# Performance work log

Measured on AMD Instinct MI355X. Metric: run time of the kernel, lower is better.

## Reference

```python
import jax, jax.numpy as jnp
import numpy as np

B, T = 32, 256
CHAR_V, BICHAR_V, CTYPE_V = 10000, 200000, 8
CD, BD, TD = 100, 100, 20
LIN, H = 200, 200
IN_DIMS = 2 * CD + 2 * BD + TD  # 420


def lstm_scan(xs, Wih, Whh, b, reverse=False):
    # xs: [T, B, LIN]; Wih: [4H, LIN]; Whh: [4H, H]; b: [4H]
    h0 = jnp.zeros((xs.shape[1], Whh.shape[1]), xs.dtype)
    c0 = jnp.zeros_like(h0)

    def step(carry, x):
        h, c = carry
        g = x @ Wih.T + h @ Whh.T + b  # [B, 4H]
        i, f, gg, o = jnp.split(g, 4, axis=-1)  # torch LSTMCell gate order
        c = jax.nn.sigmoid(f) * c + jax.nn.sigmoid(i) * jnp.tanh(gg)
        h = jax.nn.sigmoid(o) * jnp.tanh(c)
        return (h, c), h

    _, hs = jax.lax.scan(step, (h0, c0), xs, reverse=reverse)
    return hs  # [T, B, H]


def setup_inputs() -> dict:
    key = jax.random.key(0)
    ks = jax.random.split(key, 20)
    d = {
        "chars": jax.random.randint(ks[0], (B, T), 0, CHAR_V, jnp.int32),
        "left_bichar": jax.random.randint(ks[1], (B, T), 0, BICHAR_V, jnp.int32),
        "right_bichar": jax.random.randint(ks[2], (B, T), 0, BICHAR_V, jnp.int32),
        "extchars": jax.random.randint(ks[3], (B, T), 0, CHAR_V, jnp.int32),
        "extleft_bichar": jax.random.randint(ks[4], (B, T), 0, BICHAR_V, jnp.int32),
        "extright_bichar": jax.random.randint(ks[5], (B, T), 0, BICHAR_V, jnp.int32),
        "char_type": jax.random.randint(ks[6], (B, T), 0, CTYPE_V, jnp.int32),
        "E_char": jax.random.normal(ks[7], (CHAR_V, CD), jnp.float32) * 0.1,
        "E_extchar": jax.random.normal(ks[8], (CHAR_V, CD), jnp.float32) * 0.1,
        "E_bichar": jax.random.normal(ks[9], (BICHAR_V, BD), jnp.float32) * 0.1,
        "E_extbichar": jax.random.normal(ks[10], (BICHAR_V, BD), jnp.float32) * 0.1,
        "E_ctype": jax.random.normal(ks[11], (CTYPE_V, TD), jnp.float32) * 0.1,
        "fc_w": jax.random.normal(ks[12], (LIN, IN_DIMS), jnp.float32) * (1.0 / np.sqrt(IN_DIMS)),
        "fc_b": jnp.zeros((LIN,), jnp.float32),
        "Wih_l": jax.random.normal(ks[13], (4 * H, LIN), jnp.float32) * (1.0 / np.sqrt(LIN)),
        "Whh_l": jax.random.normal(ks[14], (4 * H, H), jnp.float32) * (1.0 / np.sqrt(H)),
        "b_l": jnp.zeros((4 * H,), jnp.float32),
        "Wih_r": jax.random.normal(ks[15], (4 * H, LIN), jnp.float32) * (1.0 / np.sqrt(LIN)),
        "Whh_r": jax.random.normal(ks[16], (4 * H, H), jnp.float32) * (1.0 / np.sqrt(H)),
        "b_r": jnp.zeros((4 * H,), jnp.float32),
    }
    return d


def reference(chars, left_bichar, right_bichar, extchars, extleft_bichar,
              extright_bichar, char_type, E_char, E_extchar, E_bichar,
              E_extbichar, E_ctype, fc_w, fc_b, Wih_l, Whh_l, b_l,
              Wih_r, Whh_r, b_r):
    c_e = E_char[chars]            # [B,T,CD]
    ec_e = E_extchar[extchars]
    lb_e = E_bichar[left_bichar]   # [B,T,BD]
    elb_e = E_extbichar[extleft_bichar]
    rb_e = E_bichar[right_bichar]
    erb_e = E_extbichar[extright_bichar]
    ct_e = E_ctype[char_type]      # [B,T,TD]

    left_total = jnp.concatenate([c_e, ec_e, lb_e, elb_e, ct_e], axis=2)
    right_total = jnp.concatenate([c_e, ec_e, rb_e, erb_e, ct_e], axis=2)

    left_x = jnp.tanh(left_total @ fc_w.T + fc_b).transpose(1, 0, 2)   # [T,B,LIN]
    right_x = jnp.tanh(right_total @ fc_w.T + fc_b).transpose(1, 0, 2)

    left_hs = lstm_scan(left_x, Wih_l, Whh_l, b_l, reverse=False)   # [T,B,H]
    right_hs = lstm_scan(right_x, Wih_r, Whh_r, b_r, reverse=True)  # [T,B,H]

    out = jnp.concatenate([left_hs, right_hs], axis=2).transpose(1, 0, 2)  # [B,T,2H]
    return out
```

## Files before the change

### kernel.cpp

```cpp
#include <hip/hip_runtime.h>
#include <stdint.h>

#define B_    32
#define T_    256
#define CD    100
#define BD    100
#define TD    20
#define LIN   200
#define HD    200
#define INDIM 420
#define G4    800

typedef __attribute__((ext_vector_type(8))) short bfrag8;
typedef __attribute__((ext_vector_type(4))) float f32x4v;

static __device__ __forceinline__ unsigned short f2bf(float f) {
  unsigned u = __float_as_uint(f);
  u = u + 0x7fffu + ((u >> 16) & 1u);
  return (unsigned short)(u >> 16);
}
static __device__ __forceinline__ float bf2f(unsigned short s) {
  return __uint_as_float(((unsigned)s) << 16);
}
static __device__ __forceinline__ float tanhx(float x) {
  return 1.0f - 2.0f * __builtin_amdgcn_rcpf(1.0f + __builtin_amdgcn_exp2f(x * 2.8853900817779268f));
}
static __device__ __forceinline__ float clamp40(float x) {
  return fminf(fmaxf(x, -40.0f), 40.0f);
}

static __device__ __forceinline__ void mk_hilo(float4 a, float4 b, bfrag8& hi, bfrag8& lo) {
  float q[8] = {a.x, a.y, a.z, a.w, b.x, b.y, b.z, b.w};
  #pragma unroll
  for (int j = 0; j < 8; ++j) {
    unsigned short h = f2bf(q[j]);
    hi[j] = (short)h;
    lo[j] = (short)f2bf(q[j] - bf2f(h));
  }
}
static __device__ __forceinline__ bfrag8 mk_hi(float4 a, float4 b) {
  bfrag8 r;
  float q[8] = {a.x, a.y, a.z, a.w, b.x, b.y, b.z, b.w};
  #pragma unroll
  for (int j = 0; j < 8; ++j) r[j] = (short)f2bf(q[j]);
  return r;
}

__global__ void presplit_kernel(const float* __restrict__ fc_w,
                                const float* __restrict__ Wih_l,
                                const float* __restrict__ Wih_r,
                                unsigned short* __restrict__ fcw_hi,
                                unsigned short* __restrict__ fcw_lo,
                                unsigned short* __restrict__ wih_hi,
                                unsigned short* __restrict__ wih_lo) {
  int tid = blockIdx.x * blockDim.x + threadIdx.x;
  int stride = gridDim.x * blockDim.x;
  for (int i = tid; i < 13 * 14 * 512; i += stride) {
    int j = i & 7, l = (i >> 3) & 63, f = i >> 9;
    int kt = f % 14, nt = f / 14;
    int n = nt * 16 + (l & 15);
    int k = kt * 32 + ((l >> 4) << 3) + j;
    float v = (n < LIN && k < INDIM) ? fc_w[n * INDIM + k] : 0.0f;
    unsigned short h = f2bf(v);
    fcw_hi[i] = h;
    fcw_lo[i] = f2bf(v - bf2f(h));
  }
  for (int d = 0; d < 2; ++d) {
    const float* W = d ? Wih_r : Wih_l;
    unsigned short* oh = wih_hi + (size_t)d * 179200;
    unsigned short* ol = wih_lo + (size_t)d * 179200;
    for (int i = tid; i < 50 * 7 * 512; i += stride) {
      int j = i & 7, l = (i >> 3) & 63, f = i >> 9;
      int kt = f % 7, nt = f / 7;
      int np = nt * 16 + (l & 15);
      int no = (np & 3) * 200 + (np >> 2);
      int k = kt * 32 + ((l >> 4) << 3) + j;
      float v = (k < LIN) ? W[no * LIN + k] : 0.0f;
      unsigned short h = f2bf(v);
      oh[i] = h;
      ol[i] = f2bf(v - bf2f(h));
    }
  }
}

__global__ __launch_bounds__(256) void fc_kernel(
    const int* __restrict__ chars, const int* __restrict__ left_bichar,
    const int* __restrict__ right_bichar, const int* __restrict__ extchars,
    const int* __restrict__ extleft, const int* __restrict__ extright,
    const int* __restrict__ ctype,
    const float* __restrict__ E_char, const float* __restrict__ E_extchar,
    const float* __restrict__ E_bichar, const float* __restrict__ E_extbichar,
    const float* __restrict__ E_ctype, const float* __restrict__ fc_b,
    const unsigned short* __restrict__ fcw_hi, const unsigned short* __restrict__ fcw_lo,
    float* __restrict__ x) {
  __shared__ __align__(16) float feat[32 * 452];
  int rb = blockIdx.x;
  int dir = rb >> 8;
  int t = rb & 255;
  int tid = threadIdx.x;
  const int* bi  = dir ? right_bichar : left_bichar;
  const int* ebi = dir ? extright : extleft;

  for (int cc = tid; cc < 32 * 113; cc += 256) {
    int lr = cc / 113, kc = cc - lr * 113;
    int k = kc << 2;
    float4 v = make_float4(0.f, 0.f, 0.f, 0.f);
    if (k < INDIM) {
      int id; const float* tab; int kk; int wdt;
      if (k < 100)      { id = chars[lr * T_ + t];    tab = E_char;      kk = k;       wdt = 100; }
      else if (k < 200) { id = extchars[lr * T_ + t]; tab = E_extchar;   kk = k - 100; wdt = 100; }
      else if (k < 300) { id = bi[lr * T_ + t];       tab = E_bichar;    kk = k - 200; wdt = 100; }
      else if (k < 400) { id = ebi[lr * T_ + t];      tab = E_extbichar; kk = k - 300; wdt = 100; }
      else              { id = ctype[lr * T_ + t];    tab = E_ctype;     kk = k - 400; wdt = 20;  }
      v = *reinterpret_cast<const float4*>(tab + (size_t)id * wdt + kk);
    }
    *reinterpret_cast<float4*>(&feat[lr * 452 + k]) = v;
  }
  __syncthreads();

  int w = tid >> 6, l = tid & 63;
  int lrow = l & 15, lk8 = (l >> 4) << 3;
  f32x4v acc[8];
  #pragma unroll
  for (int i = 0; i < 8; ++i) acc[i] = (f32x4v){0.f, 0.f, 0.f, 0.f};

  for (int kt = 0; kt < 14; ++kt) {
    bfrag8 ah[2], al[2];
    #pragma unroll
    for (int mt = 0; mt < 2; ++mt) {
      const float* fp = &feat[(mt * 16 + lrow) * 452 + kt * 32 + lk8];
      float4 v0 = *reinterpret_cast<const float4*>(fp);
      float4 v1 = *reinterpret_cast<const float4*>(fp + 4);
      mk_hilo(v0, v1, ah[mt], al[mt]);
    }
    #pragma unroll
    for (int s = 0; s < 4; ++s) {
      int nt = w + (s << 2);
      if (nt < 13) {
        size_t fo = ((size_t)(nt * 14 + kt) * 64 + l) * 8;
        bfrag8 bh = *reinterpret_cast<const bfrag8*>(fcw_hi + fo);
        bfrag8 bl = *reinterpret_cast<const bfrag8*>(fcw_lo + fo);
        #pragma unroll
        for (int mt = 0; mt < 2; ++mt) {
          acc[s * 2 + mt] = __builtin_amdgcn_mfma_f32_16x16x32_bf16(ah[mt], bh, acc[s * 2 + mt], 0, 0, 0);
          acc[s * 2 + mt] = __builtin_amdgcn_mfma_f32_16x16x32_bf16(al[mt], bh, acc[s * 2 + mt], 0, 0, 0);
          acc[s * 2 + mt] = __builtin_amdgcn_mfma_f32_16x16x32_bf16(ah[mt], bl, acc[s * 2 + mt], 0, 0, 0);
        }
      }
    }
  }
  int r0 = rb * 32;
  #pragma unroll
  for (int s = 0; s < 4; ++s) {
    int nt = w + (s << 2);
    if (nt < 13) {
      int n = nt * 16 + lrow;
      if (n < LIN) {
        float bias = fc_b[n];
        #pragma unroll
        for (int mt = 0; mt < 2; ++mt) {
          #pragma unroll
          for (int rr = 0; rr < 4; ++rr) {
            int row = mt * 16 + ((l >> 4) << 2) + rr;
            x[(size_t)(r0 + row) * LIN + n] = tanhx(acc[s * 2 + mt][rr] + bias);
          }
        }
      }
    }
  }
}

__global__ __launch_bounds__(512) void xwih_kernel(
    const float* __restrict__ x, const unsigned short* __restrict__ wih_hi,
    const unsigned short* __restrict__ wih_lo, const float* __restrict__ b_l,
    const float* __restrict__ b_r, float* __restrict__ pre) {
  int bid = blockIdx.x;
  int dir = (bid >= 320) ? 1 : 0;
  int rem = bid - dir * 320;
  int rbm = rem / 5, nb = rem - rbm * 5;
  int m0 = rbm * 128, n0 = nb * 160;
  int tid = threadIdx.x, w = tid >> 6, l = tid & 63;
  int lrow = l & 15, lk8 = (l >> 4) << 3;
  const float* xd = x + (size_t)dir * 8192 * LIN;
  const unsigned short* wh = wih_hi + (size_t)dir * 179200;
  const unsigned short* wl = wih_lo + (size_t)dir * 179200;
  const float* bias = dir ? b_r : b_l;

  f32x4v acc[10];
  #pragma unroll
  for (int i = 0; i < 10; ++i) acc[i] = (f32x4v){0.f, 0.f, 0.f, 0.f};

  int row = m0 + w * 16 + lrow;
  for (int kt = 0; kt < 7; ++kt) {
    int kb = kt * 32 + lk8;
    bfrag8 ah = {0,0,0,0,0,0,0,0}, al = {0,0,0,0,0,0,0,0};
    if (kb <= 192) {
      const float* fp = xd + (size_t)row * LIN + kb;
      float4 v0 = *reinterpret_cast<const float4*>(fp);
      float4 v1 = *reinterpret_cast<const float4*>(fp + 4);
      mk_hilo(v0, v1, ah, al);
    }
    #pragma unroll
    for (int nt = 0; nt < 10; ++nt) {
      int ntg = nb * 10 + nt;
      size_t fo = ((size_t)(ntg * 7 + kt) * 64 + l) * 8;
      bfrag8 bh = *reinterpret_cast<const bfrag8*>(wh + fo);
      bfrag8 bl = *reinterpret_cast<const bfrag8*>(wl + fo);
      acc[nt] = __builtin_amdgcn_mfma_f32_16x16x32_bf16(ah, bh, acc[nt], 0, 0, 0);
      acc[nt] = __builtin_amdgcn_mfma_f32_16x16x32_bf16(al, bh, acc[nt], 0, 0, 0);
      acc[nt] = __builtin_amdgcn_mfma_f32_16x16x32_bf16(ah, bl, acc[nt], 0, 0, 0);
    }
  }
  #pragma unroll
  for (int nt = 0; nt < 10; ++nt) {
    int n = n0 + nt * 16 + lrow;
    float bb = bias[(n & 3) * 200 + (n >> 2)];
    int hcol = n >> 2, g = n & 3;
    int i6 = hcol >> 5;
    int hc5 = hcol & 31;
    int wv = hc5 >> 2, lhi = hc5 & 3;
    int chunk = (i6 < 6) ? (i6 * 8 + wv) : (48 + wv);
    #pragma unroll
    for (int rr = 0; rr < 4; ++rr) {
      int r2 = m0 + w * 16 + ((l >> 4) << 2) + rr;
      int t = r2 >> 5, b32 = r2 & 31;
      int hf2 = b32 >> 4, b = b32 & 15;
      int lane = b + 16 * lhi;
      size_t dst = ((((size_t)(dir * 2 + hf2) * 256 + t) * 50 + chunk) * 64 + lane) * 4 + g;
      pre[dst] = acc[nt][rr] + bb;
    }
  }
}

__global__ __launch_bounds__(512, 2) void lstm_kernel(
    const float* __restrict__ pre, const float* __restrict__ Whh_l,
    const float* __restrict__ Whh_r, float* __restrict__ out) {
  __shared__ __align__(16) unsigned short hbufA[3584];
  __shared__ __align__(16) unsigned short hbufB[3584];
  __shared__ __align__(16) unsigned short whx[7168];
  __shared__ __align__(16) float pbuf0[12800];
  __shared__ __align__(16) float pbuf1[12800];

  int bi = blockIdx.x;
  int dir = bi >> 1, half = bi & 1;
  const float* Whh = dir ? Whh_r : Whh_l;
  int tid = threadIdx.x, w = tid >> 6, l = tid & 63;
  int lrow = l & 15, lk8 = (l >> 4) << 3;

  bfrag8 Breg[6][7];
  #pragma unroll
  for (int i = 0; i < 6; ++i) {
    int np = (w + 8 * i) * 16 + lrow;
    int no = (np & 3) * 200 + (np >> 2);
    #pragma unroll
    for (int kt = 0; kt < 7; ++kt) {
      int kb = kt * 32 + lk8;
      bfrag8 bb = {0,0,0,0,0,0,0,0};
      if (kb <= 192) {
        const float* fp = Whh + (size_t)no * HD + kb;
        bb = mk_hi(*reinterpret_cast<const float4*>(fp),
                   *reinterpret_cast<const float4*>(fp + 4));
      }
      Breg[i][kt] = bb;
    }
  }
  for (int e = tid; e < 896; e += 512) {
    int l2 = e & 63, f = e >> 6;
    int kt = f % 7, tile = f / 7;
    int np = (48 + tile) * 16 + (l2 & 15);
    int no = (np & 3) * 200 + (np >> 2);
    int kb = kt * 32 + ((l2 >> 4) << 3);
    bfrag8 bb = {0,0,0,0,0,0,0,0};
    if (kb <= 192) {
      const float* fp = Whh + (size_t)no * HD + kb;
      bb = mk_hi(*reinterpret_cast<const float4*>(fp),
                 *reinterpret_cast<const float4*>(fp + 4));
    }
    *reinterpret_cast<bfrag8*>(&whx[(size_t)e * 8]) = bb;
  }
  for (int e = tid; e < 896; e += 512) {
    reinterpret_cast<uint64_t*>(hbufA)[e] = 0;
    reinterpret_cast<uint64_t*>(hbufB)[e] = 0;
  }
  float c[7];
  #pragma unroll
  for (int i = 0; i < 7; ++i) c[i] = 0.f;

  int hbase = 4 * w + (l >> 4);
  int hw = (lrow + 16 * ((hbase >> 3) & 3)) * 8 + (hbase & 7);

  const char* psrcB = (const char*)(pre
                      + ((size_t)(dir * 2 + half) * 256 + (dir ? 255 : 0)) * 12800)
                    + w * 1024 + l * 16;
  const int pstepB = dir ? -51200 : 51200;
  float* outp = out + (size_t)((half * 16 + lrow) * 256 + (dir ? 255 : 0)) * 400
              + dir * 200 + (l >> 4) + 4 * w;
  const int ostep = dir ? -400 : 400;

  __syncthreads();

  #pragma unroll
  for (int i = 0; i < 6; ++i)
    __builtin_amdgcn_global_load_lds(
        (const __attribute__((address_space(1))) void*)(psrcB + i * 8192),
        (__attribute__((address_space(3))) void*)(&pbuf0[(8 * i + w) * 256]), 16, 0, 0);
  if (w < 2)
    __builtin_amdgcn_global_load_lds(
        (const __attribute__((address_space(1))) void*)(psrcB + 49152),
        (__attribute__((address_space(3))) void*)(&pbuf0[(48 + w) * 256]), 16, 0, 0);
  psrcB += pstepB;
  asm volatile("s_waitcnt vmcnt(0)");
  __syncthreads();

  const float NL  = -1.4426950408889634f;
  const float N2L = -2.8853900817779268f;

  auto STEP = [&](const unsigned short* rbuf, unsigned short* wbuf,
                  const float* pcur, float* pnxt) {
    #pragma unroll
    for (int i = 0; i < 6; ++i)
      __builtin_amdgcn_global_load_lds(
          (const __attribute__((address_space(1))) void*)(psrcB + i * 8192),
          (__attribute__((address_space(3))) void*)(pnxt + (8 * i + w) * 256), 16, 0, 0);
    if (w < 2)
      __builtin_amdgcn_global_load_lds(
          (const __attribute__((address_space(1))) void*)(psrcB + 49152),
          (__attribute__((address_space(3))) void*)(pnxt + (48 + w) * 256), 16, 0, 0);
    psrcB += pstepB;
    __builtin_amdgcn_sched_barrier(0x1 | 0x2 | 0x4 | 0x8);
    asm volatile("s_waitcnt vmcnt(12)");
    __builtin_amdgcn_sched_barrier(0x1 | 0x2 | 0x4 | 0x8);
    f32x4v acc[7];
    #pragma unroll
    for (int i = 0; i < 6; ++i)
      acc[i] = *reinterpret_cast<const f32x4v*>(pcur + (8 * i + w) * 256 + l * 4);
    acc[6] = (f32x4v){0.f, 0.f, 0.f, 0.f};
    if (w < 2)
      acc[6] = *reinterpret_cast<const f32x4v*>(pcur + (48 + w) * 256 + l * 4);
    #pragma unroll
    for (int kt = 0; kt < 7; ++kt) {
      bfrag8 hf = *reinterpret_cast<const bfrag8*>(&rbuf[kt * 512 + l * 8]);
      #pragma unroll
      for (int i = 0; i < 6; ++i)
        acc[i] = __builtin_amdgcn_mfma_f32_16x16x32_bf16(Breg[i][kt], hf, acc[i], 0, 0, 0);
      if (w < 2) {
        bfrag8 b6 = *reinterpret_cast<const bfrag8*>(&whx[(w * 7 + kt) * 512 + l * 8]);
        acc[6] = __builtin_amdgcn_mfma_f32_16x16x32_bf16(b6, hf, acc[6], 0, 0, 0);
      }
    }
    #pragma unroll
    for (int i = 0; i < 7; ++i) {
      if (i < 6 || w < 2) {
        float ig = acc[i][0];
        float fg = acc[i][1];
        float gg = acc[i][2];
        float og = acc[i][3];
        float u  = __builtin_amdgcn_exp2f(clamp40(fg * NL));
        float v  = __builtin_amdgcn_exp2f(clamp40(ig * NL));
        float Wt = __builtin_amdgcn_exp2f(clamp40(gg * N2L));
        float y  = __builtin_amdgcn_exp2f(clamp40(og * NL));
        float pu = 1.f + u, pv = 1.f + v, pw = 1.f + Wt, py = 1.f + y;
        float P  = pv * pw;
        float r1 = __builtin_amdgcn_rcpf(pu * P);
        float cn = (c[i] * P + pu * (1.f - Wt)) * r1;
        c[i] = cn;
        float Z  = __builtin_amdgcn_exp2f(clamp40(cn * N2L));
        float h  = (1.f - Z) * __builtin_amdgcn_rcpf(py * (1.f + Z));
        outp[32 * i] = h;
        wbuf[hw + i * 512] = f2bf(h);
      }
    }
    outp += ostep;
    __builtin_amdgcn_sched_barrier(0x1 | 0x2 | 0x4 | 0x8);
    asm volatile("s_waitcnt lgkmcnt(0)");
    __builtin_amdgcn_s_barrier();
    __builtin_amdgcn_sched_barrier(0x1 | 0x2 | 0x4 | 0x8);
  };

  for (int it = 0; it < 128; ++it) {
    STEP(hbufA, hbufB, pbuf0, pbuf1);
    STEP(hbufB, hbufA, pbuf1, pbuf0);
  }
}

extern "C" void kernel_launch(void* const* d_in, const int* in_sizes, int n_in,
                              void* d_out, int out_size, void* d_ws, size_t ws_size,
                              hipStream_t stream) {
  (void)in_sizes; (void)n_in; (void)out_size; (void)ws_size;
  const int* chars        = (const int*)d_in[0];
  const int* left_bichar  = (const int*)d_in[1];
  const int* right_bichar = (const int*)d_in[2];
  const int* extchars     = (const int*)d_in[3];
  const int* extleft      = (const int*)d_in[4];
  const int* extright     = (const int*)d_in[5];
  const int* ctype        = (const int*)d_in[6];
  const float* E_char      = (const float*)d_in[7];
  const float* E_extchar   = (const float*)d_in[8];
  const float* E_bichar    = (const float*)d_in[9];
  const float* E_extbichar = (const float*)d_in[10];
  const float* E_ctype     = (const float*)d_in[11];
  const float* fc_w  = (const float*)d_in[12];
  const float* fc_b  = (const float*)d_in[13];
  const float* Wih_l = (const float*)d_in[14];
  const float* Whh_l = (const float*)d_in[15];
  const float* b_l   = (const float*)d_in[16];
  const float* Wih_r = (const float*)d_in[17];
  const float* Whh_r = (const float*)d_in[18];
  const float* b_r   = (const float*)d_in[19];
  float* out = (float*)d_out;
  char* ws = (char*)d_ws;

  float* x   = (float*)(ws);
  float* pre = (float*)(ws + 13107200);
  unsigned short* fcw_hi = (unsigned short*)(ws + 65536000);
  unsigned short* fcw_lo = (unsigned short*)(ws + 65722368);
  unsigned short* wih_hi = (unsigned short*)(ws + 65908736);
  unsigned short* wih_lo = (unsigned short*)(ws + 66625536);

  presplit_kernel<<<256, 256, 0, stream>>>(fc_w, Wih_l, Wih_r, fcw_hi, fcw_lo, wih_hi, wih_lo);
  fc_kernel<<<512, 256, 0, stream>>>(chars, left_bichar, right_bichar, extchars,
                                     extleft, extright, ctype, E_char, E_extchar,
                                     E_bichar, E_extbichar, E_ctype, fc_b,
                                     fcw_hi, fcw_lo, x);
  xwih_kernel<<<640, 512, 0, stream>>>(x, wih_hi, wih_lo, b_l, b_r, pre);
  lstm_kernel<<<4, 512, 0, stream>>>(pre, Whh_l, Whh_r, out);
}
```

Measured before the change: 766.0 us.

## Double LSTM recurrence block to 1024 threads, halving per-wave gate tiles

Raises the recurrent LSTM kernel from 8 to 16 waves per block, so each wave owns 3 gate tiles (plus the remainder tile on two waves) instead of 6. The precomputed-gate layout in the input-projection kernel, the LDS prefetch addressing, the vmcnt waits and the h write-back indexing are all remapped to match. The aim is to shorten the serial per-timestep critical path by spreading the MFMA and activation work over more waves. In exchange, each barrier now synchronises 16 waves and the remainder tiles on waves 0-1 are a larger share of the per-step work.

```diff
diff --git a/kernel.cpp b/kernel.cpp
--- a/kernel.cpp
+++ b/kernel.cpp
@@ -216,23 +216,21 @@
     int n = n0 + nt * 16 + lrow;
     float bb = bias[(n & 3) * 200 + (n >> 2)];
     int hcol = n >> 2, g = n & 3;
-    int i6 = hcol >> 5;
-    int hc5 = hcol & 31;
-    int wv = hc5 >> 2, lhi = hc5 & 3;
-    int chunk = (i6 < 6) ? (i6 * 8 + wv) : (48 + wv);
+    int tau = hcol >> 2;
+    int lhi = hcol & 3;
     #pragma unroll
     for (int rr = 0; rr < 4; ++rr) {
       int r2 = m0 + w * 16 + ((l >> 4) << 2) + rr;
       int t = r2 >> 5, b32 = r2 & 31;
       int hf2 = b32 >> 4, b = b32 & 15;
       int lane = b + 16 * lhi;
-      size_t dst = ((((size_t)(dir * 2 + hf2) * 256 + t) * 50 + chunk) * 64 + lane) * 4 + g;
+      size_t dst = ((((size_t)(dir * 2 + hf2) * 256 + t) * 50 + tau) * 64 + lane) * 4 + g;
       pre[dst] = acc[nt][rr] + bb;
     }
   }
 }
 
-__global__ __launch_bounds__(512, 2) void lstm_kernel(
+__global__ __launch_bounds__(1024, 1) void lstm_kernel(
     const float* __restrict__ pre, const float* __restrict__ Whh_l,
     const float* __restrict__ Whh_r, float* __restrict__ out) {
   __shared__ __align__(16) unsigned short hbufA[3584];
@@ -246,11 +244,12 @@
   const float* Whh = dir ? Whh_r : Whh_l;
   int tid = threadIdx.x, w = tid >> 6, l = tid & 63;
   int lrow = l & 15, lk8 = (l >> 4) << 3;
-
-  bfrag8 Breg[6][7];
-  #pragma unroll
-  for (int i = 0; i < 6; ++i) {
-    int np = (w + 8 * i) * 16 + lrow;
+  int hl = l >> 4;
+
+  bfrag8 Breg[3][7];
+  #pragma unroll
+  for (int i = 0; i < 3; ++i) {
+    int np = (w + 16 * i) * 16 + lrow;
     int no = (np & 3) * 200 + (np >> 2);
     #pragma unroll
     for (int kt = 0; kt < 7; ++kt) {
@@ -264,7 +263,7 @@
       Breg[i][kt] = bb;
     }
   }
-  for (int e = tid; e < 896; e += 512) {
+  for (int e = tid; e < 896; e += 1024) {
     int l2 = e & 63, f = e >> 6;
     int kt = f % 7, tile = f / 7;
     int np = (48 + tile) * 16 + (l2 & 15);
@@ -278,35 +277,32 @@
     }
     *reinterpret_cast<bfrag8*>(&whx[(size_t)e * 8]) = bb;
   }
-  for (int e = tid; e < 896; e += 512) {
+  for (int e = tid; e < 896; e += 1024) {
     reinterpret_cast<uint64_t*>(hbufA)[e] = 0;
     reinterpret_cast<uint64_t*>(hbufB)[e] = 0;
   }
-  float c[7];
-  #pragma unroll
-  for (int i = 0; i < 7; ++i) c[i] = 0.f;
-
-  int hbase = 4 * w + (l >> 4);
-  int hw = (lrow + 16 * ((hbase >> 3) & 3)) * 8 + (hbase & 7);
+  float c[4];
+  #pragma unroll
+  for (int i = 0; i < 4; ++i) c[i] = 0.f;
 
   const char* psrcB = (const char*)(pre
                       + ((size_t)(dir * 2 + half) * 256 + (dir ? 255 : 0)) * 12800)
-                    + w * 1024 + l * 16;
+                    + l * 16;
   const int pstepB = dir ? -51200 : 51200;
   float* outp = out + (size_t)((half * 16 + lrow) * 256 + (dir ? 255 : 0)) * 400
-              + dir * 200 + (l >> 4) + 4 * w;
+              + dir * 200 + 4 * w + hl;
   const int ostep = dir ? -400 : 400;
 
   __syncthreads();
 
   #pragma unroll
-  for (int i = 0; i < 6; ++i)
+  for (int i = 0; i < 3; ++i)
     __builtin_amdgcn_global_load_lds(
-        (const __attribute__((address_space(1))) void*)(psrcB + i * 8192),
-        (__attribute__((address_space(3))) void*)(&pbuf0[(8 * i + w) * 256]), 16, 0, 0);
+        (const __attribute__((address_space(1))) void*)(psrcB + (w + 16 * i) * 1024),
+        (__attribute__((address_space(3))) void*)(&pbuf0[(w + 16 * i) * 256]), 16, 0, 0);
   if (w < 2)
     __builtin_amdgcn_global_load_lds(
-        (const __attribute__((address_space(1))) void*)(psrcB + 49152),
+        (const __attribute__((address_space(1))) void*)(psrcB + (48 + w) * 1024),
         (__attribute__((address_space(3))) void*)(&pbuf0[(48 + w) * 256]), 16, 0, 0);
   psrcB += pstepB;
   asm volatile("s_waitcnt vmcnt(0)");
@@ -318,39 +314,40 @@
   auto STEP = [&](const unsigned short* rbuf, unsigned short* wbuf,
                   const float* pcur, float* pnxt) {
     #pragma unroll
-    for (int i = 0; i < 6; ++i)
+    for (int i = 0; i < 3; ++i)
       __builtin_amdgcn_global_load_lds(
-          (const __attribute__((address_space(1))) void*)(psrcB + i * 8192),
-          (__attribute__((address_space(3))) void*)(pnxt + (8 * i + w) * 256), 16, 0, 0);
+          (const __attribute__((address_space(1))) void*)(psrcB + (w + 16 * i) * 1024),
+          (__attribute__((address_space(3))) void*)(pnxt + (w + 16 * i) * 256), 16, 0, 0);
     if (w < 2)
       __builtin_amdgcn_global_load_lds(
-          (const __attribute__((address_space(1))) void*)(psrcB + 49152),
+          (const __attribute__((address_space(1))) void*)(psrcB + (48 + w) * 1024),
           (__attribute__((address_space(3))) void*)(pnxt + (48 + w) * 256), 16, 0, 0);
     psrcB += pstepB;
     __builtin_amdgcn_sched_barrier(0x1 | 0x2 | 0x4 | 0x8);
-    asm volatile("s_waitcnt vmcnt(12)");
+    if (w < 2) { asm volatile("s_waitcnt vmcnt(8)"); }
+    else       { asm volatile("s_waitcnt vmcnt(6)"); }
     __builtin_amdgcn_sched_barrier(0x1 | 0x2 | 0x4 | 0x8);
-    f32x4v acc[7];
-    #pragma unroll
-    for (int i = 0; i < 6; ++i)
-      acc[i] = *reinterpret_cast<const f32x4v*>(pcur + (8 * i + w) * 256 + l * 4);
-    acc[6] = (f32x4v){0.f, 0.f, 0.f, 0.f};
+    f32x4v acc[4];
+    #pragma unroll
+    for (int i = 0; i < 3; ++i)
+      acc[i] = *reinterpret_cast<const f32x4v*>(pcur + (w + 16 * i) * 256 + l * 4);
+    acc[3] = (f32x4v){0.f, 0.f, 0.f, 0.f};
     if (w < 2)
-      acc[6] = *reinterpret_cast<const f32x4v*>(pcur + (48 + w) * 256 + l * 4);
+      acc[3] = *reinterpret_cast<const f32x4v*>(pcur + (48 + w) * 256 + l * 4);
     #pragma unroll
     for (int kt = 0; kt < 7; ++kt) {
       bfrag8 hf = *reinterpret_cast<const bfrag8*>(&rbuf[kt * 512 + l * 8]);
       #pragma unroll
-      for (int i = 0; i < 6; ++i)
+      for (int i = 0; i < 3; ++i)
         acc[i] = __builtin_amdgcn_mfma_f32_16x16x32_bf16(Breg[i][kt], hf, acc[i], 0, 0, 0);
       if (w < 2) {
         bfrag8 b6 = *reinterpret_cast<const bfrag8*>(&whx[(w * 7 + kt) * 512 + l * 8]);
-        acc[6] = __builtin_amdgcn_mfma_f32_16x16x32_bf16(b6, hf, acc[6], 0, 0, 0);
+        acc[3] = __builtin_amdgcn_mfma_f32_16x16x32_bf16(b6, hf, acc[3], 0, 0, 0);
       }
     }
     #pragma unroll
-    for (int i = 0; i < 7; ++i) {
-      if (i < 6 || w < 2) {
+    for (int i = 0; i < 4; ++i) {
+      if (i < 3 || w < 2) {
         float ig = acc[i][0];
         float fg = acc[i][1];
         float gg = acc[i][2];
@@ -366,8 +363,10 @@
         c[i] = cn;
         float Z  = __builtin_amdgcn_exp2f(clamp40(cn * N2L));
         float h  = (1.f - Z) * __builtin_amdgcn_rcpf(py * (1.f + Z));
-        outp[32 * i] = h;
-        wbuf[hw + i * 512] = f2bf(h);
+        outp[64 * i] = h;
+        int hcol = 4 * w + 64 * i + hl;
+        int kth = hcol >> 5, k5 = hcol & 31;
+        wbuf[kth * 512 + (lrow + ((k5 >> 3) << 4)) * 8 + (k5 & 7)] = f2bf(h);
       }
     }
     outp += ostep;
@@ -423,5 +422,5 @@
                                      E_bichar, E_extbichar, E_ctype, fc_b,
                                      fcw_hi, fcw_lo, x);
   xwih_kernel<<<640, 512, 0, stream>>>(x, wih_hi, wih_lo, b_l, b_r, pre);
-  lstm_kernel<<<4, 512, 0, stream>>>(pre, Whh_l, Whh_r, out);
-}
+  lstm_kernel<<<4, 1024, 0, stream>>>(pre, Whh_l, Whh_r, out);
+}
```

Measured after the change: 929.2 us. 1.21x slower.

## Interleave per-tile MFMA chains with gate math and reorder precompute layout

Applied to the files above, without the earlier changes.

Reorders the recurrent step so each output tile's MFMA chain over the 7 k-slices is followed immediately by its gate nonlinearities. This lets the transcendental math of one tile overlap with the matrix work of the next, instead of finishing all MFMAs before any gate math. The h fragments are preloaded into registers and the block is raised to priority 1 around the compute. The precomputed-gate layout is changed so each wave's chunk index maps directly to tau, and the vmcnt wait is adjusted for waves that issue an extra load. The risk is longer dependent MFMA chains per tile with less independent accumulation to hide MFMA latency.

```diff
diff --git a/kernel.cpp b/kernel.cpp
--- a/kernel.cpp
+++ b/kernel.cpp
@@ -216,17 +216,15 @@
     int n = n0 + nt * 16 + lrow;
     float bb = bias[(n & 3) * 200 + (n >> 2)];
     int hcol = n >> 2, g = n & 3;
-    int i6 = hcol >> 5;
-    int hc5 = hcol & 31;
-    int wv = hc5 >> 2, lhi = hc5 & 3;
-    int chunk = (i6 < 6) ? (i6 * 8 + wv) : (48 + wv);
+    int tau = hcol >> 2;
+    int lhi = hcol & 3;
     #pragma unroll
     for (int rr = 0; rr < 4; ++rr) {
       int r2 = m0 + w * 16 + ((l >> 4) << 2) + rr;
       int t = r2 >> 5, b32 = r2 & 31;
       int hf2 = b32 >> 4, b = b32 & 15;
       int lane = b + 16 * lhi;
-      size_t dst = ((((size_t)(dir * 2 + hf2) * 256 + t) * 50 + chunk) * 64 + lane) * 4 + g;
+      size_t dst = ((((size_t)(dir * 2 + hf2) * 256 + t) * 50 + tau) * 64 + lane) * 4 + g;
       pre[dst] = acc[nt][rr] + bb;
     }
   }
@@ -291,7 +289,7 @@
 
   const char* psrcB = (const char*)(pre
                       + ((size_t)(dir * 2 + half) * 256 + (dir ? 255 : 0)) * 12800)
-                    + w * 1024 + l * 16;
+                    + l * 16;
   const int pstepB = dir ? -51200 : 51200;
   float* outp = out + (size_t)((half * 16 + lrow) * 256 + (dir ? 255 : 0)) * 400
               + dir * 200 + (l >> 4) + 4 * w;
@@ -302,11 +300,11 @@
   #pragma unroll
   for (int i = 0; i < 6; ++i)
     __builtin_amdgcn_global_load_lds(
-        (const __attribute__((address_space(1))) void*)(psrcB + i * 8192),
+        (const __attribute__((address_space(1))) void*)(psrcB + (8 * i + w) * 1024),
         (__attribute__((address_space(3))) void*)(&pbuf0[(8 * i + w) * 256]), 16, 0, 0);
   if (w < 2)
     __builtin_amdgcn_global_load_lds(
-        (const __attribute__((address_space(1))) void*)(psrcB + 49152),
+        (const __attribute__((address_space(1))) void*)(psrcB + (48 + w) * 1024),
         (__attribute__((address_space(3))) void*)(&pbuf0[(48 + w) * 256]), 16, 0, 0);
   psrcB += pstepB;
   asm volatile("s_waitcnt vmcnt(0)");
@@ -320,45 +318,38 @@
     #pragma unroll
     for (int i = 0; i < 6; ++i)
       __builtin_amdgcn_global_load_lds(
-          (const __attribute__((address_space(1))) void*)(psrcB + i * 8192),
+          (const __attribute__((address_space(1))) void*)(psrcB + (8 * i + w) * 1024),
           (__attribute__((address_space(3))) void*)(pnxt + (8 * i + w) * 256), 16, 0, 0);
     if (w < 2)
       __builtin_amdgcn_global_load_lds(
-          (const __attribute__((address_space(1))) void*)(psrcB + 49152),
+          (const __attribute__((address_space(1))) void*)(psrcB + (48 + w) * 1024),
           (__attribute__((address_space(3))) void*)(pnxt + (48 + w) * 256), 16, 0, 0);
     psrcB += pstepB;
     __builtin_amdgcn_sched_barrier(0x1 | 0x2 | 0x4 | 0x8);
-    asm volatile("s_waitcnt vmcnt(12)");
+    if (w < 2) { asm volatile("s_waitcnt vmcnt(14)"); }
+    else       { asm volatile("s_waitcnt vmcnt(12)"); }
     __builtin_amdgcn_sched_barrier(0x1 | 0x2 | 0x4 | 0x8);
-    f32x4v acc[7];
-    #pragma unroll
-    for (int i = 0; i < 6; ++i)
-      acc[i] = *reinterpret_cast<const f32x4v*>(pcur + (8 * i + w) * 256 + l * 4);
-    acc[6] = (f32x4v){0.f, 0.f, 0.f, 0.f};
-    if (w < 2)
-      acc[6] = *reinterpret_cast<const f32x4v*>(pcur + (48 + w) * 256 + l * 4);
-    #pragma unroll
-    for (int kt = 0; kt < 7; ++kt) {
-      bfrag8 hf = *reinterpret_cast<const bfrag8*>(&rbuf[kt * 512 + l * 8]);
-      #pragma unroll
-      for (int i = 0; i < 6; ++i)
-        acc[i] = __builtin_amdgcn_mfma_f32_16x16x32_bf16(Breg[i][kt], hf, acc[i], 0, 0, 0);
-      if (w < 2) {
-        bfrag8 b6 = *reinterpret_cast<const bfrag8*>(&whx[(w * 7 + kt) * 512 + l * 8]);
-        acc[6] = __builtin_amdgcn_mfma_f32_16x16x32_bf16(b6, hf, acc[6], 0, 0, 0);
-      }
-    }
+    bfrag8 hf[7];
+    #pragma unroll
+    for (int kt = 0; kt < 7; ++kt)
+      hf[kt] = *reinterpret_cast<const bfrag8*>(&rbuf[kt * 512 + l * 8]);
+    __builtin_amdgcn_s_setprio(1);
     #pragma unroll
     for (int i = 0; i < 7; ++i) {
       if (i < 6 || w < 2) {
-        float ig = acc[i][0];
-        float fg = acc[i][1];
-        float gg = acc[i][2];
-        float og = acc[i][3];
-        float u  = __builtin_amdgcn_exp2f(clamp40(fg * NL));
-        float v  = __builtin_amdgcn_exp2f(clamp40(ig * NL));
-        float Wt = __builtin_amdgcn_exp2f(clamp40(gg * N2L));
-        float y  = __builtin_amdgcn_exp2f(clamp40(og * NL));
+        int tau = (i < 6) ? (8 * i + w) : (48 + w);
+        f32x4v a = *reinterpret_cast<const f32x4v*>(pcur + tau * 256 + l * 4);
+        #pragma unroll
+        for (int kt = 0; kt < 7; ++kt) {
+          bfrag8 bb;
+          if (i < 6) bb = Breg[i][kt];
+          else       bb = *reinterpret_cast<const bfrag8*>(&whx[(w * 7 + kt) * 512 + l * 8]);
+          a = __builtin_amdgcn_mfma_f32_16x16x32_bf16(bb, hf[kt], a, 0, 0, 0);
+        }
+        float u  = __builtin_amdgcn_exp2f(clamp40(a[1] * NL));
+        float v  = __builtin_amdgcn_exp2f(clamp40(a[0] * NL));
+        float Wt = __builtin_amdgcn_exp2f(clamp40(a[2] * N2L));
+        float y  = __builtin_amdgcn_exp2f(clamp40(a[3] * NL));
         float pu = 1.f + u, pv = 1.f + v, pw = 1.f + Wt, py = 1.f + y;
         float P  = pv * pw;
         float r1 = __builtin_amdgcn_rcpf(pu * P);
@@ -370,6 +361,7 @@
         wbuf[hw + i * 512] = f2bf(h);
       }
     }
+    __builtin_amdgcn_s_setprio(0);
     outp += ostep;
     __builtin_amdgcn_sched_barrier(0x1 | 0x2 | 0x4 | 0x8);
     asm volatile("s_waitcnt lgkmcnt(0)");
```

Result: faster. 663.9 us, median of 3 (-13.3%).
